# Kernel optimization log

Hardware: AMD Instinct MI355X
Metric: run time of the kernel (lower is better)

Reference implementation:

```python
import jax, jax.numpy as jnp
import numpy as np

H = 256      # hidden_units
NB = 2       # num_blocks
NH = 4       # num_heads
E = 8        # num_experts
K = 2        # top_k
L = 200      # maxlen
B = 128      # batch
ITEM = 100000
USER = 50000


def _ln(x, w, b, eps):
    m = x.mean(-1, keepdims=True)
    v = ((x - m) ** 2).mean(-1, keepdims=True)
    return (x - m) / jnp.sqrt(v + eps) * w + b


def setup_inputs() -> dict:
    key = jax.random.key(0)
    ks = iter(jax.random.split(key, 48))

    def n(shape, s=0.02):
        return jax.random.normal(next(ks), shape, jnp.float32) * s

    item_emb = n((ITEM + 1, H)).at[0].set(0.0)   # padding_idx=0
    pos_emb = n((L + 1, H)).at[0].set(0.0)
    user_emb = n((USER + 1, H)).at[0].set(0.0)
    return dict(
        user_ids=jax.random.randint(next(ks), (B,), 1, USER + 1),
        log_seqs=jax.random.randint(next(ks), (B, L), 0, ITEM + 1),
        item_ids=jax.random.randint(next(ks), (B,), 1, ITEM + 1),
        item_emb=item_emb, pos_emb=pos_emb, user_emb=user_emb,
        ln1_w=jnp.ones((NB, H)), ln1_b=jnp.zeros((NB, H)),
        inproj_w=n((NB, 3 * H, H)), inproj_b=jnp.zeros((NB, 3 * H)),
        outproj_w=n((NB, H, H)), outproj_b=jnp.zeros((NB, H)),
        ln2_w=jnp.ones((NB, H)), ln2_b=jnp.zeros((NB, H)),
        gate_w=n((NB, E, H)), gate_b=jnp.zeros((NB, E)),
        e_w1=n((NB, E, H, H)), e_b1=jnp.zeros((NB, E, H)),
        e_w2=n((NB, E, H, H)), e_b2=jnp.zeros((NB, E, H)),
        moeln_w=jnp.ones((NB, H)), moeln_b=jnp.zeros((NB, H)),
        lastln_w=jnp.ones((H,)), lastln_b=jnp.zeros((H,)),
    )


def reference(user_ids, log_seqs, item_ids, item_emb, pos_emb, user_emb,
              ln1_w, ln1_b, inproj_w, inproj_b, outproj_w, outproj_b,
              ln2_w, ln2_b, gate_w, gate_b, e_w1, e_b1, e_w2, e_b2,
              moeln_w, moeln_b, lastln_w, lastln_b):
    hd = H // NH
    # embeddings (padding id 0 -> zero rows)
    x = item_emb[log_seqs] * jnp.sqrt(jnp.float32(H))          # [B,L,H]
    poss = jnp.arange(1, L + 1)[None, :] * (log_seqs != 0)      # 0 where padded
    x = x + pos_emb[poss]
    causal = jnp.tril(jnp.ones((L, L), bool))

    for i in range(NB):
        # pre-LN query, raw x as key/value (matches original)
        q_in = _ln(x, ln1_w[i], ln1_b[i], 1e-8)
        wq, wk, wv = jnp.split(inproj_w[i], 3, axis=0)
        bq, bk, bv = jnp.split(inproj_b[i], 3)
        q = (q_in @ wq.T + bq).reshape(B, L, NH, hd)
        k = (x @ wk.T + bk).reshape(B, L, NH, hd)
        v = (x @ wv.T + bv).reshape(B, L, NH, hd)
        s = jnp.einsum('bqnd,bknd->bnqk', q, k) / jnp.sqrt(jnp.float32(hd))
        s = jnp.where(causal, s, -jnp.inf)
        a = jax.nn.softmax(s, axis=-1)
        ctx = jnp.einsum('bnqk,bknd->bqnd', a, v).reshape(B, L, H)
        mha = ctx @ outproj_w[i].T + outproj_b[i]
        x = q_in + mha
        x = _ln(x, ln2_w[i], ln2_b[i], 1e-8)

        # SparseMoE: top-k gate, all-expert dense compute, masked combine
        gl = jnp.einsum('bsh,eh->bse', x, gate_w[i]) + gate_b[i]
        w, idx = jax.lax.top_k(gl, K)
        w = jax.nn.softmax(w, axis=-1)
        comb = (jax.nn.one_hot(idx, E) * w[..., None]).sum(-2)   # [B,L,E]
        h = jax.nn.relu(jnp.einsum('bsh,ehd->besd', x, e_w1[i])
                        + e_b1[i][None, :, None, :])              # [B,E,L,H]
        y = jnp.einsum('besd,edh->besh', h, e_w2[i]) + e_b2[i][None, :, None, :]
        moe = jnp.einsum('bse,besh->bsh', comb, y)
        x = _ln(x + moe, moeln_w[i], moeln_b[i], 1e-5)

    x = _ln(x, lastln_w, lastln_b, 1e-8)
    final = x[:, -1, :] + user_emb[user_ids]
    return (final * item_emb[item_ids]).sum(-1)   # [B] logits
```

## Files before the change

### kernel.cpp

```cpp
#include <hip/hip_runtime.h>
#include <math.h>

#define H 256
#define NHEAD 4
#define HD 64
#define NEXP 8
#define SEQL 200
#define BATCH 128
#define NF (BATCH*SEQL)
#define KT 64
#define QT 32
#define QW 8

__device__ __forceinline__ float blk_sum256(float v, float* s4) {
    #pragma unroll
    for (int o = 32; o > 0; o >>= 1) v += __shfl_xor(v, o, 64);
    __syncthreads();
    if ((threadIdx.x & 63) == 0) s4[threadIdx.x >> 6] = v;
    __syncthreads();
    return s4[0] + s4[1] + s4[2] + s4[3];
}

__global__ __launch_bounds__(256) void embed_kernel(
    const int* __restrict__ seqs, const float* __restrict__ item_emb,
    const float* __restrict__ pos_emb, float* __restrict__ x)
{
    int n = blockIdx.x, t = threadIdx.x;
    int id = seqs[n];
    int pos = (id != 0) ? (n % SEQL) + 1 : 0;
    x[(size_t)n*H + t] = item_emb[(size_t)id*H + t] * 16.0f + pos_emb[(size_t)pos*H + t];
}

__global__ __launch_bounds__(256) void ln_kernel(
    const float* __restrict__ in, const float* __restrict__ res,
    float* __restrict__ out, const float* __restrict__ w, const float* __restrict__ b,
    float eps, int base, int step)
{
    __shared__ float s4[4];
    int r = blockIdx.x, t = threadIdx.x;
    float v = in[(size_t)(base + r*step)*H + t];
    if (res) v += res[(size_t)r*H + t];
    float mean = blk_sum256(v, s4) * (1.f/H);
    float d = v - mean;
    float var = blk_sum256(d*d, s4) * (1.f/H);
    out[(size_t)r*H + t] = d * rsqrtf(var + eps) * w[t] + b[t];
}

__global__ __launch_bounds__(256) void moe_ln_kernel(
    const float* __restrict__ x, const float* __restrict__ ybuf,
    const int* __restrict__ tok_pair, const float* __restrict__ top_w,
    float* __restrict__ out, const float* __restrict__ w, const float* __restrict__ b,
    float eps)
{
    __shared__ float s4[4];
    int r = blockIdx.x, t = threadIdx.x;
    int p0 = tok_pair[r*2], p1 = tok_pair[r*2+1];
    float v = x[(size_t)r*H + t]
            + top_w[r*2+0] * ybuf[(size_t)p0*H + t]
            + top_w[r*2+1] * ybuf[(size_t)p1*H + t];
    float mean = blk_sum256(v, s4) * (1.f/H);
    float d = v - mean;
    float var = blk_sum256(d*d, s4) * (1.f/H);
    out[(size_t)r*H + t] = d * rsqrtf(var + eps) * w[t] + b[t];
}

__global__ __launch_bounds__(256) void gemm_nt(
    const float* __restrict__ A, const float* __restrict__ W,
    const float* __restrict__ bias, float* __restrict__ out, int nrows)
{
    __shared__ float As[16][68];
    __shared__ float Ws[16][68];
    int r0 = blockIdx.x * 64;
    if (r0 >= nrows) return;
    int c0 = blockIdx.y * 64;
    int tid = threadIdx.x;
    int tx = tid & 15, ty = tid >> 4;
    int lrow = tid >> 2, lkg = (tid & 3) << 2;
    float acc[4][4] = {};
    for (int kk = 0; kk < H; kk += 16) {
        float4 av = make_float4(0.f,0.f,0.f,0.f);
        int gr = r0 + lrow;
        if (gr < nrows) av = *(const float4*)(A + (size_t)gr*H + kk + lkg);
        As[lkg+0][lrow]=av.x; As[lkg+1][lrow]=av.y; As[lkg+2][lrow]=av.z; As[lkg+3][lrow]=av.w;
        float4 wv = *(const float4*)(W + (size_t)(c0+lrow)*H + kk + lkg);
        Ws[lkg+0][lrow]=wv.x; Ws[lkg+1][lrow]=wv.y; Ws[lkg+2][lrow]=wv.z; Ws[lkg+3][lrow]=wv.w;
        __syncthreads();
        #pragma unroll
        for (int k = 0; k < 16; ++k) {
            float4 a = *(const float4*)&As[k][ty<<2];
            float4 bv = *(const float4*)&Ws[k][tx<<2];
            float aa[4] = {a.x,a.y,a.z,a.w};
            float bb[4] = {bv.x,bv.y,bv.z,bv.w};
            #pragma unroll
            for (int ii = 0; ii < 4; ++ii)
                #pragma unroll
                for (int jj = 0; jj < 4; ++jj)
                    acc[ii][jj] += aa[ii] * bb[jj];
        }
        __syncthreads();
    }
    #pragma unroll
    for (int ii = 0; ii < 4; ++ii) {
        int gr = r0 + (ty<<2) + ii;
        if (gr < nrows) {
            #pragma unroll
            for (int jj = 0; jj < 4; ++jj) {
                int gc = c0 + (tx<<2) + jj;
                out[(size_t)gr*H + gc] = acc[ii][jj] + bias[gc];
            }
        }
    }
}

template<int GATHER, int RELU, int BT>
__device__ __forceinline__ void gemm128_body(
    const float* __restrict__ A, const float* __restrict__ W,
    const float* __restrict__ bias, float* __restrict__ out, int nrows,
    const int* __restrict__ pair_tok)
{
    __shared__ float As[16][132];
    __shared__ float Ws[16][132];
    int r0 = blockIdx.x * 128;
    if (r0 >= nrows) return;
    int c0 = blockIdx.y * 128;
    int tid = threadIdx.x;
    int tx = tid & 15, ty = tid >> 4;
    int lrow = tid >> 1, lkg = (tid & 1) << 3;
    int ar = r0 + lrow;
    bool va = ar < nrows;
    int ga = ar;
    if (GATHER) ga = va ? pair_tok[r0 + lrow] : 0;
    const float* ap = A + (size_t)(va ? ga : 0)*H + lkg;
    const float* wpT = W + (size_t)(c0 + lrow)*H + lkg;
    int kr0 = tid >> 5, cg = (tid & 31) << 2;
    const float* wpN0 = W + (size_t)kr0*H + c0 + cg;
    const float* wpN1 = wpN0 + (size_t)8*H;
    float acc[8][8] = {};
    for (int kk = 0; kk < H; kk += 16) {
        float4 av0 = make_float4(0.f,0.f,0.f,0.f), av1 = av0;
        if (va) { av0 = *(const float4*)(ap + kk); av1 = *(const float4*)(ap + kk + 4); }
        float4 wv0, wv1;
        if (BT) {
            wv0 = *(const float4*)(wpT + kk);
            wv1 = *(const float4*)(wpT + kk + 4);
        } else {
            wv0 = *(const float4*)(wpN0 + (size_t)kk*H);
            wv1 = *(const float4*)(wpN1 + (size_t)kk*H);
        }
        __syncthreads();
        As[lkg+0][lrow]=av0.x; As[lkg+1][lrow]=av0.y; As[lkg+2][lrow]=av0.z; As[lkg+3][lrow]=av0.w;
        As[lkg+4][lrow]=av1.x; As[lkg+5][lrow]=av1.y; As[lkg+6][lrow]=av1.z; As[lkg+7][lrow]=av1.w;
        if (BT) {
            Ws[lkg+0][lrow]=wv0.x; Ws[lkg+1][lrow]=wv0.y; Ws[lkg+2][lrow]=wv0.z; Ws[lkg+3][lrow]=wv0.w;
            Ws[lkg+4][lrow]=wv1.x; Ws[lkg+5][lrow]=wv1.y; Ws[lkg+6][lrow]=wv1.z; Ws[lkg+7][lrow]=wv1.w;
        } else {
            *(float4*)&Ws[kr0][cg]     = wv0;
            *(float4*)&Ws[kr0 + 8][cg] = wv1;
        }
        __syncthreads();
        #pragma unroll
        for (int k = 0; k < 16; ++k) {
            float4 a0 = *(const float4*)&As[k][ty<<2];
            float4 a1 = *(const float4*)&As[k][64 + (ty<<2)];
            float4 b0 = *(const float4*)&Ws[k][tx<<2];
            float4 b1 = *(const float4*)&Ws[k][64 + (tx<<2)];
            float aa[8] = {a0.x,a0.y,a0.z,a0.w,a1.x,a1.y,a1.z,a1.w};
            float bb[8] = {b0.x,b0.y,b0.z,b0.w,b1.x,b1.y,b1.z,b1.w};
            #pragma unroll
            for (int ii = 0; ii < 8; ++ii)
                #pragma unroll
                for (int jj = 0; jj < 8; ++jj)
                    acc[ii][jj] += aa[ii] * bb[jj];
        }
    }
    #pragma unroll
    for (int hr = 0; hr < 2; ++hr)
        #pragma unroll
        for (int ii = 0; ii < 4; ++ii) {
            int row = r0 + 64*hr + (ty<<2) + ii;
            if (row < nrows) {
                #pragma unroll
                for (int hc = 0; hc < 2; ++hc) {
                    int col = c0 + 64*hc + (tx<<2);
                    #pragma unroll
                    for (int jj = 0; jj < 4; ++jj) {
                        float o = acc[4*hr+ii][4*hc+jj] + bias[col+jj];
                        if (RELU) o = fmaxf(o, 0.f);
                        out[(size_t)row*H + col + jj] = o;
                    }
                }
            }
        }
}

__global__ __launch_bounds__(256) void gemm_nt128(
    const float* __restrict__ A, const float* __restrict__ W,
    const float* __restrict__ bias, float* __restrict__ out, int nrows)
{
    gemm128_body<0,0,1>(A, W, bias, out, nrows, nullptr);
}

__global__ __launch_bounds__(256) void moe1_128(
    const float* __restrict__ X, const float* __restrict__ W1base,
    const float* __restrict__ b1base, const int* __restrict__ pair_tok,
    const int* __restrict__ offsets, const int* __restrict__ counts,
    float* __restrict__ hbuf)
{
    int e = blockIdx.z;
    int cnt = counts[e], off = offsets[e];
    gemm128_body<1,1,0>(X, W1base + (size_t)e*H*H, b1base + (size_t)e*H,
                        hbuf + (size_t)off*H, cnt, pair_tok + off);
}

__global__ __launch_bounds__(256) void moe2_128(
    const float* __restrict__ Hbuf, const float* __restrict__ W2base,
    const float* __restrict__ b2base, const int* __restrict__ offsets,
    const int* __restrict__ counts, float* __restrict__ ybuf)
{
    int e = blockIdx.z;
    int cnt = counts[e], off = offsets[e];
    gemm128_body<0,0,0>(Hbuf + (size_t)off*H, W2base + (size_t)e*H*H, b2base + (size_t)e*H,
                        ybuf + (size_t)off*H, cnt, nullptr);
}

__global__ __launch_bounds__(256) void attn_kernel(
    const float* __restrict__ qbuf, const float* __restrict__ kbuf,
    const float* __restrict__ vbuf, float* __restrict__ ctx, int nq)
{
    __shared__ float Ks[KT][HD+4];
    __shared__ float VsT[HD][KT+4];
    __shared__ float qs[QT][HD+4];
    __shared__ float ps[QT][KT+4];
    int b = blockIdx.x, h = blockIdx.y, z = blockIdx.z;
    int qbase = z * QT;
    int nqt = nq - qbase;
    if (nqt <= 0) return;
    if (nqt > QT) nqt = QT;
    int tid = threadIdx.x, w = tid >> 6, lane = tid & 63;
    int off = SEQL - nq;
    for (int i = tid; i < QT*(HD/4); i += 256) {
        int row = i >> 4, c4 = (i & 15) << 2;
        float4 qv = make_float4(0.f,0.f,0.f,0.f);
        if (row < nqt) qv = *(const float4*)(qbuf + (size_t)(b*nq + qbase + row)*H + h*HD + c4);
        *(float4*)&qs[row][c4] = qv;
    }
    float m[QW], l[QW], acc[QW];
    #pragma unroll
    for (int i = 0; i < QW; ++i) { m[i] = -3e30f; l[i] = 0.f; acc[i] = 0.f; }
    int wq0 = w * QW;
    int wqn = nqt - wq0; if (wqn > QW) wqn = QW;
    int wmaxpos = qbase + wq0 + (wqn > 0 ? wqn - 1 : 0) + off;
    int ntiles = (qbase + nqt - 1 + off) / KT + 1;
    int q_sub = lane >> 3, kq = lane & 7;
    for (int t = 0; t < ntiles; ++t) {
        int kbase = t * KT;
        __syncthreads();
        for (int i = tid; i < KT*(HD/4); i += 256) {
            int row = i >> 4, c4 = (i & 15) << 2;
            int key = kbase + row;
            float4 kv = make_float4(0.f,0.f,0.f,0.f);
            if (key < SEQL) kv = *(const float4*)(kbuf + (size_t)(b*SEQL + key)*H + h*HD + c4);
            *(float4*)&Ks[row][c4] = kv;
        }
        {
            int key = kbase + lane;
            bool kval = key < SEQL;
            const float* vp = vbuf + (size_t)(b*SEQL + (kval ? key : 0))*H + h*HD;
            #pragma unroll
            for (int it = 0; it < 4; ++it) {
                int c4 = ((it << 2) + w) << 2;
                float4 vv = make_float4(0.f,0.f,0.f,0.f);
                if (kval) vv = *(const float4*)(vp + c4);
                VsT[c4+0][lane] = vv.x; VsT[c4+1][lane] = vv.y;
                VsT[c4+2][lane] = vv.z; VsT[c4+3][lane] = vv.w;
            }
        }
        __syncthreads();
        if (wqn > 0 && kbase <= wmaxpos) {
            float s[QW];
            #pragma unroll
            for (int qi = 0; qi < QW; ++qi) s[qi] = 0.f;
            #pragma unroll 4
            for (int d4 = 0; d4 < HD; d4 += 4) {
                float4 k4 = *(const float4*)&Ks[lane][d4];
                #pragma unroll
                for (int qi = 0; qi < QW; ++qi) {
                    float4 q4 = *(const float4*)&qs[wq0+qi][d4];
                    s[qi] += k4.x*q4.x + k4.y*q4.y + k4.z*q4.z + k4.w*q4.w;
                }
            }
            #pragma unroll
            for (int qi = 0; qi < QW; ++qi) {
                if (qi < wqn) {
                    int qpos = qbase + wq0 + qi + off;
                    bool valid = (kbase + lane) <= qpos;
                    ps[wq0+qi][lane] = valid ? s[qi]*0.125f : -3e30f;
                }
            }
            float mq = m[0];
            #pragma unroll
            for (int i = 1; i < QW; ++i) if (q_sub == i) mq = m[i];
            const float2* pr = (const float2*)&ps[wq0+q_sub][kq*8];
            float2 a0 = pr[0], a1 = pr[1], a2 = pr[2], a3 = pr[3];
            float mloc = fmaxf(fmaxf(fmaxf(a0.x,a0.y), fmaxf(a1.x,a1.y)),
                               fmaxf(fmaxf(a2.x,a2.y), fmaxf(a3.x,a3.y)));
            float tm = mloc;
            #pragma unroll
            for (int o = 1; o < 8; o <<= 1) tm = fmaxf(tm, __shfl_xor(tm, o, 64));
            float mn = fmaxf(mq, tm);
            float p0 = expf(a0.x-mn), p1 = expf(a0.y-mn), p2 = expf(a1.x-mn), p3 = expf(a1.y-mn);
            float p4 = expf(a2.x-mn), p5 = expf(a2.y-mn), p6 = expf(a3.x-mn), p7 = expf(a3.y-mn);
            float psum = ((p0+p1)+(p2+p3)) + ((p4+p5)+(p6+p7));
            #pragma unroll
            for (int o = 1; o < 8; o <<= 1) psum += __shfl_xor(psum, o, 64);
            float2* pw = (float2*)&ps[wq0+q_sub][kq*8];
            pw[0] = make_float2(p0,p1); pw[1] = make_float2(p2,p3);
            pw[2] = make_float2(p4,p5); pw[3] = make_float2(p6,p7);
            #pragma unroll
            for (int qi = 0; qi < QW; ++qi) {
                float tmv = __shfl(tm, qi*8, 64);
                float psv = __shfl(psum, qi*8, 64);
                if (qi < wqn) {
                    float mn2 = fmaxf(m[qi], tmv);
                    float scl = expf(m[qi] - mn2);
                    l[qi] = l[qi]*scl + psv;
                    acc[qi] *= scl;
                    m[qi] = mn2;
                }
            }
            #pragma unroll 4
            for (int k4 = 0; k4 < KT; k4 += 4) {
                float4 v4 = *(const float4*)&VsT[lane][k4];
                #pragma unroll
                for (int qi = 0; qi < QW; ++qi) {
                    if (qi < wqn) {
                        float4 p4v = *(const float4*)&ps[wq0+qi][k4];
                        acc[qi] += p4v.x*v4.x + p4v.y*v4.y + p4v.z*v4.z + p4v.w*v4.w;
                    }
                }
            }
        }
    }
    #pragma unroll
    for (int qi = 0; qi < QW; ++qi) {
        if (qi < wqn) {
            ctx[(size_t)(b*nq + qbase + wq0 + qi)*H + h*HD + lane] = acc[qi] / l[qi];
        }
    }
}

__global__ __launch_bounds__(256) void gate_kernel(
    const float* __restrict__ X, const float* __restrict__ gw, const float* __restrict__ gb,
    int* __restrict__ top_idx, float* __restrict__ top_w, int nrows)
{
    __shared__ float gl[NEXP];
    int n = blockIdx.x;
    int tid = threadIdx.x;
    int wv = tid >> 6, lane = tid & 63;
    float xv[4];
    #pragma unroll
    for (int c = 0; c < 4; ++c) xv[c] = X[(size_t)n*H + lane + (c<<6)];
    #pragma unroll
    for (int s = 0; s < 2; ++s) {
        int e = wv*2 + s;
        float acc = 0.f;
        #pragma unroll
        for (int c = 0; c < 4; ++c) acc += xv[c] * gw[(size_t)e*H + lane + (c<<6)];
        #pragma unroll
        for (int o = 32; o > 0; o >>= 1) acc += __shfl_xor(acc, o, 64);
        if (lane == 0) gl[e] = acc + gb[e];
    }
    __syncthreads();
    if (tid == 0) {
        int i0 = 0;
        for (int e = 1; e < NEXP; ++e) if (gl[e] > gl[i0]) i0 = e;
        int i1 = -1;
        for (int e = 0; e < NEXP; ++e) { if (e == i0) continue; if (i1 < 0 || gl[e] > gl[i1]) i1 = e; }
        float e1 = expf(gl[i1] - gl[i0]);
        float w0 = 1.f / (1.f + e1);
        top_idx[n*2+0] = i0; top_idx[n*2+1] = i1;
        top_w[n*2+0] = w0;  top_w[n*2+1] = 1.f - w0;
    }
}

__global__ __launch_bounds__(256) void count_kernel(
    const int* __restrict__ top_idx, int* __restrict__ counts, int nrows)
{
    __shared__ int hist[NEXP];
    int tid = threadIdx.x;
    if (tid < NEXP) hist[tid] = 0;
    __syncthreads();
    int n = blockIdx.x * 256 + tid;
    if (n < nrows) {
        atomicAdd(&hist[top_idx[n*2+0]], 1);
        atomicAdd(&hist[top_idx[n*2+1]], 1);
    }
    __syncthreads();
    if (tid < NEXP && hist[tid] > 0) atomicAdd(&counts[tid], hist[tid]);
}

__global__ void scan_kernel(const int* __restrict__ counts, int* __restrict__ offsets,
                            int* __restrict__ cursor)
{
    int s = 0;
    for (int e = 0; e < NEXP; ++e) { offsets[e] = s; cursor[e] = s; s += counts[e]; }
}

__global__ __launch_bounds__(256) void scatter_kernel(
    const int* __restrict__ top_idx,
    int* __restrict__ cursor, int* __restrict__ pair_tok, int* __restrict__ tok_pair, int nrows)
{
    __shared__ int lcnt[NEXP];
    __shared__ int lbase[NEXP];
    int tid = threadIdx.x;
    if (tid < NEXP) lcnt[tid] = 0;
    __syncthreads();
    int n = blockIdx.x * 256 + tid;
    int e0 = 0, e1 = 0, p0 = 0, p1 = 0;
    bool act = n < nrows;
    if (act) {
        e0 = top_idx[n*2+0]; e1 = top_idx[n*2+1];
        p0 = atomicAdd(&lcnt[e0], 1);
        p1 = atomicAdd(&lcnt[e1], 1);
    }
    __syncthreads();
    if (tid < NEXP) lbase[tid] = (lcnt[tid] > 0) ? atomicAdd(&cursor[tid], lcnt[tid]) : 0;
    __syncthreads();
    if (act) {
        int q0 = lbase[e0] + p0, q1 = lbase[e1] + p1;
        pair_tok[q0] = n; pair_tok[q1] = n;
        tok_pair[n*2+0] = q0; tok_pair[n*2+1] = q1;
    }
}

__global__ __launch_bounds__(256) void moe_gemm1(
    const float* __restrict__ X, const float* __restrict__ W1base,
    const float* __restrict__ b1base, const int* __restrict__ pair_tok,
    const int* __restrict__ offsets, const int* __restrict__ counts,
    float* __restrict__ hbuf)
{
    int e = blockIdx.z;
    int cnt = counts[e];
    int r0 = blockIdx.x * 64;
    if (r0 >= cnt) return;
    int off = offsets[e];
    int c0 = blockIdx.y * 64;
    const float* W = W1base + (size_t)e * H * H;
    const float* bias = b1base + (size_t)e * H;
    __shared__ float As[16][68];
    __shared__ float Bs[16][68];
    int tid = threadIdx.x, tx = tid & 15, ty = tid >> 4;
    int lrow = tid >> 2, lkg = (tid & 3) << 2;
    float acc[4][4] = {};
    for (int kk = 0; kk < H; kk += 16) {
        float4 av = make_float4(0.f,0.f,0.f,0.f);
        int pr = r0 + lrow;
        if (pr < cnt) {
            int tok = pair_tok[off + pr];
            av = *(const float4*)(X + (size_t)tok*H + kk + lkg);
        }
        As[lkg+0][lrow]=av.x; As[lkg+1][lrow]=av.y; As[lkg+2][lrow]=av.z; As[lkg+3][lrow]=av.w;
        float4 wv = *(const float4*)(W + (size_t)(kk+ty)*H + c0 + (tx<<2));
        *(float4*)&Bs[ty][tx<<2] = wv;
        __syncthreads();
        #pragma unroll
        for (int k = 0; k < 16; ++k) {
            float4 a = *(const float4*)&As[k][ty<<2];
            float4 bv = *(const float4*)&Bs[k][tx<<2];
            float aa[4] = {a.x,a.y,a.z,a.w};
            float bb[4] = {bv.x,bv.y,bv.z,bv.w};
            #pragma unroll
            for (int ii = 0; ii < 4; ++ii)
                #pragma unroll
                for (int jj = 0; jj < 4; ++jj)
                    acc[ii][jj] += aa[ii] * bb[jj];
        }
        __syncthreads();
    }
    #pragma unroll
    for (int ii = 0; ii < 4; ++ii) {
        int pr = r0 + (ty<<2) + ii;
        if (pr < cnt) {
            #pragma unroll
            for (int jj = 0; jj < 4; ++jj) {
                int gc = c0 + (tx<<2) + jj;
                hbuf[(size_t)(off+pr)*H + gc] = fmaxf(acc[ii][jj] + bias[gc], 0.f);
            }
        }
    }
}

__global__ __launch_bounds__(256) void moe_gemm2(
    const float* __restrict__ Hbuf, const float* __restrict__ W2base,
    const float* __restrict__ b2base, const int* __restrict__ offsets,
    const int* __restrict__ counts, float* __restrict__ ybuf)
{
    int e = blockIdx.z;
    int cnt = counts[e];
    int r0 = blockIdx.x * 64;
    if (r0 >= cnt) return;
    int off = offsets[e];
    int c0 = blockIdx.y * 64;
    const float* W = W2base + (size_t)e * H * H;
    const float* bias = b2base + (size_t)e * H;
    __shared__ float As[16][68];
    __shared__ float Bs[16][68];
    int tid = threadIdx.x, tx = tid & 15, ty = tid >> 4;
    int lrow = tid >> 2, lkg = (tid & 3) << 2;
    float acc[4][4] = {};
    for (int kk = 0; kk < H; kk += 16) {
        float4 av = make_float4(0.f,0.f,0.f,0.f);
        int pr = r0 + lrow;
        if (pr < cnt) av = *(const float4*)(Hbuf + (size_t)(off+pr)*H + kk + lkg);
        As[lkg+0][lrow]=av.x; As[lkg+1][lrow]=av.y; As[lkg+2][lrow]=av.z; As[lkg+3][lrow]=av.w;
        float4 wv = *(const float4*)(W + (size_t)(kk+ty)*H + c0 + (tx<<2));
        *(float4*)&Bs[ty][tx<<2] = wv;
        __syncthreads();
        #pragma unroll
        for (int k = 0; k < 16; ++k) {
            float4 a = *(const float4*)&As[k][ty<<2];
            float4 bv = *(const float4*)&Bs[k][tx<<2];
            float aa[4] = {a.x,a.y,a.z,a.w};
            float bb[4] = {bv.x,bv.y,bv.z,bv.w};
            #pragma unroll
            for (int ii = 0; ii < 4; ++ii)
                #pragma unroll
                for (int jj = 0; jj < 4; ++jj)
                    acc[ii][jj] += aa[ii] * bb[jj];
        }
        __syncthreads();
    }
    #pragma unroll
    for (int ii = 0; ii < 4; ++ii) {
        int pr = r0 + (ty<<2) + ii;
        if (pr < cnt) {
            #pragma unroll
            for (int jj = 0; jj < 4; ++jj) {
                int gc = c0 + (tx<<2) + jj;
                ybuf[(size_t)(off+pr)*H + gc] = acc[ii][jj] + bias[gc];
            }
        }
    }
}

__global__ void zero_kernel(float* __restrict__ p, int n) {
    int i = blockIdx.x * 256 + threadIdx.x;
    if (i < n) p[i] = 0.f;
}

__global__ __launch_bounds__(256) void final_kernel(
    const float* __restrict__ xf, const float* __restrict__ lnw, const float* __restrict__ lnb,
    const float* __restrict__ user_emb, const float* __restrict__ item_emb,
    const int* __restrict__ user_ids, const int* __restrict__ item_ids, float* __restrict__ out)
{
    __shared__ float s4[4];
    int bb = blockIdx.x, t = threadIdx.x;
    float v = xf[(size_t)bb*H + t];
    float mean = blk_sum256(v, s4) * (1.f/H);
    float d = v - mean;
    float var = blk_sum256(d*d, s4) * (1.f/H);
    float lnv = d * rsqrtf(var + 1e-8f) * lnw[t] + lnb[t];
    float fin = lnv + user_emb[(size_t)user_ids[bb]*H + t];
    float prod = fin * item_emb[(size_t)item_ids[bb]*H + t];
    float tot = blk_sum256(prod, s4);
    if (t == 0) out[bb] = tot;
}

extern "C" void kernel_launch(void* const* d_in, const int* in_sizes, int n_in,
                              void* d_out, int out_size, void* d_ws, size_t ws_size,
                              hipStream_t stream)
{
    (void)in_sizes; (void)n_in; (void)out_size; (void)ws_size;
    const int*   user_ids  = (const int*)d_in[0];
    const int*   log_seqs  = (const int*)d_in[1];
    const int*   item_ids  = (const int*)d_in[2];
    const float* item_emb  = (const float*)d_in[3];
    const float* pos_emb   = (const float*)d_in[4];
    const float* user_emb  = (const float*)d_in[5];
    const float* ln1_w     = (const float*)d_in[6];
    const float* ln1_b     = (const float*)d_in[7];
    const float* inproj_w  = (const float*)d_in[8];
    const float* inproj_b  = (const float*)d_in[9];
    const float* outproj_w = (const float*)d_in[10];
    const float* outproj_b = (const float*)d_in[11];
    const float* ln2_w     = (const float*)d_in[12];
    const float* ln2_b     = (const float*)d_in[13];
    const float* gate_w    = (const float*)d_in[14];
    const float* gate_b    = (const float*)d_in[15];
    const float* e_w1      = (const float*)d_in[16];
    const float* e_b1      = (const float*)d_in[17];
    const float* e_w2      = (const float*)d_in[18];
    const float* e_b2      = (const float*)d_in[19];
    const float* moeln_w   = (const float*)d_in[20];
    const float* moeln_b   = (const float*)d_in[21];
    const float* lastln_w  = (const float*)d_in[22];
    const float* lastln_b  = (const float*)d_in[23];

    float* ws = (float*)d_ws;
    const size_t NFH = (size_t)NF * H;
    float* buf0 = ws;
    float* buf1 = buf0 + NFH;
    float* buf2 = buf1 + NFH;
    float* buf3 = buf2 + NFH;
    float* buf4 = buf3 + NFH;
    float* s0   = buf4 + NFH;
    float* s1   = s0 + (size_t)BATCH*H;
    float* s2   = s1 + (size_t)BATCH*H;
    float* s3   = s2 + (size_t)BATCH*H;
    float* s6   = s3 + (size_t)BATCH*H;
    float* s4   = s6 + (size_t)BATCH*H;
    float* s5   = s4 + (size_t)2*BATCH*H;
    float* top_w   = s5 + (size_t)2*BATCH*H;
    int*   top_idx = (int*)(top_w + (size_t)NF*2);
    int*   pair_tok= top_idx + (size_t)NF*2;
    int*   tok_pair= pair_tok + (size_t)NF*2;
    int*   counts  = tok_pair + (size_t)NF*2;
    int*   offsets = counts + NEXP;
    int*   cursor  = offsets + NEXP;

    dim3 blk(256);
    dim3 g128((NF+127)/128, H/128);
    dim3 gsmall((BATCH+63)/64, H/64);
    dim3 m128((NF+127)/128, H/128, NEXP);
    dim3 msmall((BATCH+63)/64, H/64, NEXP);

    embed_kernel<<<NF, blk, 0, stream>>>(log_seqs, item_emb, pos_emb, buf0);

    {
        const int i = 0;
        const float* Wq = inproj_w + (size_t)i*3*H*H;
        const float* Wk = Wq + (size_t)H*H;
        const float* Wv = Wk + (size_t)H*H;
        const float* bq = inproj_b + (size_t)i*3*H;
        ln_kernel<<<NF, blk, 0, stream>>>(buf0, nullptr, buf1, ln1_w + i*H, ln1_b + i*H, 1e-8f, 0, 1);
        gemm_nt128<<<g128, blk, 0, stream>>>(buf1, Wq, bq,       buf2, NF);
        gemm_nt128<<<g128, blk, 0, stream>>>(buf0, Wk, bq + H,   buf3, NF);
        gemm_nt128<<<g128, blk, 0, stream>>>(buf0, Wv, bq + 2*H, buf4, NF);
        attn_kernel<<<dim3(BATCH, NHEAD, (SEQL+QT-1)/QT), blk, 0, stream>>>(buf2, buf3, buf4, buf2, SEQL);
        gemm_nt128<<<g128, blk, 0, stream>>>(buf2, outproj_w + (size_t)i*H*H, outproj_b + i*H, buf3, NF);
        ln_kernel<<<NF, blk, 0, stream>>>(buf1, buf3, buf0, ln2_w + i*H, ln2_b + i*H, 1e-8f, 0, 1);
        zero_kernel<<<1, 32, 0, stream>>>((float*)counts, NEXP);
        gate_kernel<<<NF, blk, 0, stream>>>(buf0, gate_w + (size_t)i*NEXP*H, gate_b + i*NEXP,
                                            top_idx, top_w, NF);
        count_kernel<<<(NF+255)/256, blk, 0, stream>>>(top_idx, counts, NF);
        scan_kernel<<<1, 1, 0, stream>>>(counts, offsets, cursor);
        scatter_kernel<<<(NF+255)/256, blk, 0, stream>>>(top_idx, cursor, pair_tok, tok_pair, NF);
        moe1_128<<<m128, blk, 0, stream>>>(buf0, e_w1 + (size_t)i*NEXP*H*H, e_b1 + (size_t)i*NEXP*H,
                                           pair_tok, offsets, counts, buf3);
        moe2_128<<<m128, blk, 0, stream>>>(buf3, e_w2 + (size_t)i*NEXP*H*H, e_b2 + (size_t)i*NEXP*H,
                                           offsets, counts, buf1);
        moe_ln_kernel<<<NF, blk, 0, stream>>>(buf0, buf1, tok_pair, top_w, buf3,
                                              moeln_w + i*H, moeln_b + i*H, 1e-5f);
    }

    {
        const int i = 1;
        const float* Wq = inproj_w + (size_t)i*3*H*H;
        const float* Wk = Wq + (size_t)H*H;
        const float* Wv = Wk + (size_t)H*H;
        const float* bq = inproj_b + (size_t)i*3*H;
        float* X = buf3;
        ln_kernel<<<BATCH, blk, 0, stream>>>(X, nullptr, s0, ln1_w + i*H, ln1_b + i*H, 1e-8f, SEQL-1, SEQL);
        gemm_nt<<<gsmall, blk, 0, stream>>>(s0, Wq, bq, s1, BATCH);
        gemm_nt128<<<g128, blk, 0, stream>>>(X, Wk, bq + H,   buf0, NF);
        gemm_nt128<<<g128, blk, 0, stream>>>(X, Wv, bq + 2*H, buf1, NF);
        attn_kernel<<<dim3(BATCH, NHEAD, 1), blk, 0, stream>>>(s1, buf0, buf1, s2, 1);
        gemm_nt<<<gsmall, blk, 0, stream>>>(s2, outproj_w + (size_t)i*H*H, outproj_b + i*H, s3, BATCH);
        ln_kernel<<<BATCH, blk, 0, stream>>>(s0, s3, s2, ln2_w + i*H, ln2_b + i*H, 1e-8f, 0, 1);
        zero_kernel<<<1, 32, 0, stream>>>((float*)counts, NEXP);
        gate_kernel<<<BATCH, blk, 0, stream>>>(s2, gate_w + (size_t)i*NEXP*H, gate_b + i*NEXP,
                                               top_idx, top_w, BATCH);
        count_kernel<<<1, blk, 0, stream>>>(top_idx, counts, BATCH);
        scan_kernel<<<1, 1, 0, stream>>>(counts, offsets, cursor);
        scatter_kernel<<<1, blk, 0, stream>>>(top_idx, cursor, pair_tok, tok_pair, BATCH);
        moe_gemm1<<<msmall, blk, 0, stream>>>(s2, e_w1 + (size_t)i*NEXP*H*H, e_b1 + (size_t)i*NEXP*H,
                                              pair_tok, offsets, counts, s4);
        moe_gemm2<<<msmall, blk, 0, stream>>>(s4, e_w2 + (size_t)i*NEXP*H*H, e_b2 + (size_t)i*NEXP*H,
                                              offsets, counts, s5);
        moe_ln_kernel<<<BATCH, blk, 0, stream>>>(s2, s5, tok_pair, top_w, s6,
                                                 moeln_w + i*H, moeln_b + i*H, 1e-5f);
    }

    final_kernel<<<BATCH, blk, 0, stream>>>(s6, lastln_w, lastln_b, user_emb, item_emb,
                                            user_ids, item_ids, (float*)d_out);
}
```

Before: 902.5 us.

## Double attention query tile to 64 with 512 threads and shared K/V buffer

The attention kernel's query tile grows from 32 to 64 rows and runs with 512 threads (8 waves), so each K/V tile loaded from global memory serves twice as many queries. K and V now share a single LDS buffer. V is loaded transposed only after the score phase, which adds two extra block barriers per key tile. This cuts global K/V traffic and LDS footprint per query. In exchange it adds synchronisation, leaves fewer blocks in the grid, and wastes more work in the last partial query tile (200 is not a multiple of 64).

```diff
diff --git a/kernel.cpp b/kernel.cpp
--- a/kernel.cpp
+++ b/kernel.cpp
@@ -9,7 +9,7 @@
 #define BATCH 128
 #define NF (BATCH*SEQL)
 #define KT 64
-#define QT 32
+#define QT 64
 #define QW 8
 
 __device__ __forceinline__ float blk_sum256(float v, float* s4) {
@@ -223,12 +223,11 @@
                         ybuf + (size_t)off*H, cnt, nullptr);
 }
 
-__global__ __launch_bounds__(256) void attn_kernel(
+__global__ __launch_bounds__(512) void attn_kernel(
     const float* __restrict__ qbuf, const float* __restrict__ kbuf,
     const float* __restrict__ vbuf, float* __restrict__ ctx, int nq)
 {
-    __shared__ float Ks[KT][HD+4];
-    __shared__ float VsT[HD][KT+4];
+    __shared__ float kv[KT*(HD+4)];
     __shared__ float qs[QT][HD+4];
     __shared__ float ps[QT][KT+4];
     int b = blockIdx.x, h = blockIdx.y, z = blockIdx.z;
@@ -238,7 +237,7 @@
     if (nqt > QT) nqt = QT;
     int tid = threadIdx.x, w = tid >> 6, lane = tid & 63;
     int off = SEQL - nq;
-    for (int i = tid; i < QT*(HD/4); i += 256) {
+    for (int i = tid; i < QT*(HD/4); i += 512) {
         int row = i >> 4, c4 = (i & 15) << 2;
         float4 qv = make_float4(0.f,0.f,0.f,0.f);
         if (row < nqt) qv = *(const float4*)(qbuf + (size_t)(b*nq + qbase + row)*H + h*HD + c4);
@@ -254,35 +253,23 @@
     int q_sub = lane >> 3, kq = lane & 7;
     for (int t = 0; t < ntiles; ++t) {
         int kbase = t * KT;
-        __syncthreads();
-        for (int i = tid; i < KT*(HD/4); i += 256) {
+        bool active = (wqn > 0) && (kbase <= wmaxpos);
+        __syncthreads();
+        for (int i = tid; i < KT*(HD/4); i += 512) {
             int row = i >> 4, c4 = (i & 15) << 2;
             int key = kbase + row;
-            float4 kv = make_float4(0.f,0.f,0.f,0.f);
-            if (key < SEQL) kv = *(const float4*)(kbuf + (size_t)(b*SEQL + key)*H + h*HD + c4);
-            *(float4*)&Ks[row][c4] = kv;
-        }
-        {
-            int key = kbase + lane;
-            bool kval = key < SEQL;
-            const float* vp = vbuf + (size_t)(b*SEQL + (kval ? key : 0))*H + h*HD;
-            #pragma unroll
-            for (int it = 0; it < 4; ++it) {
-                int c4 = ((it << 2) + w) << 2;
-                float4 vv = make_float4(0.f,0.f,0.f,0.f);
-                if (kval) vv = *(const float4*)(vp + c4);
-                VsT[c4+0][lane] = vv.x; VsT[c4+1][lane] = vv.y;
-                VsT[c4+2][lane] = vv.z; VsT[c4+3][lane] = vv.w;
-            }
-        }
-        __syncthreads();
-        if (wqn > 0 && kbase <= wmaxpos) {
+            float4 kvv = make_float4(0.f,0.f,0.f,0.f);
+            if (key < SEQL) kvv = *(const float4*)(kbuf + (size_t)(b*SEQL + key)*H + h*HD + c4);
+            *(float4*)&kv[row*(HD+4) + c4] = kvv;
+        }
+        __syncthreads();
+        if (active) {
             float s[QW];
             #pragma unroll
             for (int qi = 0; qi < QW; ++qi) s[qi] = 0.f;
             #pragma unroll 4
             for (int d4 = 0; d4 < HD; d4 += 4) {
-                float4 k4 = *(const float4*)&Ks[lane][d4];
+                float4 k4 = *(const float4*)&kv[lane*(HD+4) + d4];
                 #pragma unroll
                 for (int qi = 0; qi < QW; ++qi) {
                     float4 q4 = *(const float4*)&qs[wq0+qi][d4];
@@ -297,6 +284,25 @@
                     ps[wq0+qi][lane] = valid ? s[qi]*0.125f : -3e30f;
                 }
             }
+        }
+        __syncthreads();
+        {
+            int key = kbase + lane;
+            bool kval = key < SEQL;
+            const float* vp = vbuf + (size_t)(b*SEQL + (kval ? key : 0))*H + h*HD;
+            #pragma unroll
+            for (int it = 0; it < 2; ++it) {
+                int c4 = ((it << 3) + w) << 2;
+                float4 vv = make_float4(0.f,0.f,0.f,0.f);
+                if (kval) vv = *(const float4*)(vp + c4);
+                kv[(c4+0)*(KT+4) + lane] = vv.x;
+                kv[(c4+1)*(KT+4) + lane] = vv.y;
+                kv[(c4+2)*(KT+4) + lane] = vv.z;
+                kv[(c4+3)*(KT+4) + lane] = vv.w;
+            }
+        }
+        __syncthreads();
+        if (active) {
             float mq = m[0];
             #pragma unroll
             for (int i = 1; i < QW; ++i) if (q_sub == i) mq = m[i];
@@ -330,7 +336,7 @@
             }
             #pragma unroll 4
             for (int k4 = 0; k4 < KT; k4 += 4) {
-                float4 v4 = *(const float4*)&VsT[lane][k4];
+                float4 v4 = *(const float4*)&kv[lane*(KT+4) + k4];
                 #pragma unroll
                 for (int qi = 0; qi < QW; ++qi) {
                     if (qi < wqn) {
@@ -619,6 +625,7 @@
     int*   cursor  = offsets + NEXP;
 
     dim3 blk(256);
+    dim3 ablk(512);
     dim3 g128((NF+127)/128, H/128);
     dim3 gsmall((BATCH+63)/64, H/64);
     dim3 m128((NF+127)/128, H/128, NEXP);
@@ -636,7 +643,7 @@
         gemm_nt128<<<g128, blk, 0, stream>>>(buf1, Wq, bq,       buf2, NF);
         gemm_nt128<<<g128, blk, 0, stream>>>(buf0, Wk, bq + H,   buf3, NF);
         gemm_nt128<<<g128, blk, 0, stream>>>(buf0, Wv, bq + 2*H, buf4, NF);
-        attn_kernel<<<dim3(BATCH, NHEAD, (SEQL+QT-1)/QT), blk, 0, stream>>>(buf2, buf3, buf4, buf2, SEQL);
+        attn_kernel<<<dim3(BATCH, NHEAD, (SEQL+QT-1)/QT), ablk, 0, stream>>>(buf2, buf3, buf4, buf2, SEQL);
         gemm_nt128<<<g128, blk, 0, stream>>>(buf2, outproj_w + (size_t)i*H*H, outproj_b + i*H, buf3, NF);
         ln_kernel<<<NF, blk, 0, stream>>>(buf1, buf3, buf0, ln2_w + i*H, ln2_b + i*H, 1e-8f, 0, 1);
         zero_kernel<<<1, 32, 0, stream>>>((float*)counts, NEXP);
@@ -664,7 +671,7 @@
         gemm_nt<<<gsmall, blk, 0, stream>>>(s0, Wq, bq, s1, BATCH);
         gemm_nt128<<<g128, blk, 0, stream>>>(X, Wk, bq + H,   buf0, NF);
         gemm_nt128<<<g128, blk, 0, stream>>>(X, Wv, bq + 2*H, buf1, NF);
-        attn_kernel<<<dim3(BATCH, NHEAD, 1), blk, 0, stream>>>(s1, buf0, buf1, s2, 1);
+        attn_kernel<<<dim3(BATCH, NHEAD, 1), ablk, 0, stream>>>(s1, buf0, buf1, s2, 1);
         gemm_nt<<<gsmall, blk, 0, stream>>>(s2, outproj_w + (size_t)i*H*H, outproj_b + i*H, s3, BATCH);
         ln_kernel<<<BATCH, blk, 0, stream>>>(s0, s3, s2, ln2_w + i*H, ln2_b + i*H, 1e-8f, 0, 1);
         zero_kernel<<<1, 32, 0, stream>>>((float*)counts, NEXP);
```

After: 885.7 us. Within noise of the previous version (-1.9%).
